# Kernel optimization log

Measured on AMD Instinct MI355X. Metric: run time of the kernel, lower is better.

Reference implementation:

```python
import jax, jax.numpy as jnp
import numpy as np
import math

D = 64          # emb_size
R = 32          # num relations
MAX_LEN = 5000  # position table size
E = 30000       # num edges / relation instances
EPSILON = 0.01
THETA = 0.01


def _build_Q():
    # sinusoidal axes [MAX_LEN, D]
    position = jnp.arange(MAX_LEN, dtype=jnp.float32)[:, None]
    div_term = jnp.exp(jnp.arange(0, D, 2, dtype=jnp.float32) * (-math.log(10000.0) / D))
    axes = jnp.zeros((MAX_LEN, D), dtype=jnp.float32)
    axes = axes.at[:, 0::2].set(jnp.sin(position * div_term))
    axes = axes.at[:, 1::2].set(jnp.cos(position * div_term))
    # skew-symmetric generator S_ij = theta * (a_i - a_j); Q = expm(S)  [MAX_LEN, D, D]
    S = THETA * (axes[..., None] - axes[:, None, :])
    Q = jax.scipy.linalg.expm(S)
    return Q


def setup_inputs() -> dict:
    key = jax.random.key(0)
    k1, k2, k3, k4, k5 = jax.random.split(key, 5)
    std = 1.0 / jnp.sqrt(jnp.float32(D))
    relation_embs = jax.random.normal(k1, (R, D, D), dtype=jnp.float32) * std
    Q = _build_Q()
    relation_mapping = jax.random.randint(k2, (E, 2), 0, 2 * R, dtype=jnp.int64 if jax.config.jax_enable_x64 else jnp.int32)
    node_mapping = jax.random.randint(k3, (MAX_LEN,), 0, MAX_LEN)
    edge_index = jax.random.randint(k4, (2, E), 0, MAX_LEN)
    node_embs = jax.random.normal(k5, (MAX_LEN, D), dtype=jnp.float32)
    return {
        "relation_mapping": relation_mapping,
        "node_mapping": node_mapping,
        "edge_index": edge_index,
        "node_embs": node_embs,
        "relation_embs": relation_embs,
        "Q": Q,
    }


def reference(relation_mapping, node_mapping, edge_index, node_embs, relation_embs, Q):
    # node_mapping, edge_index, node_embs are unused by the original forward
    I = jnp.eye(D, dtype=relation_embs.dtype)
    W_even = I + EPSILON * relation_embs   # [R, D, D]
    W_odd = I - EPSILON * relation_embs    # [R, D, D]
    # interleave -> W[2r] = W_even[r], W[2r+1] = W_odd[r]   [2R, D, D]
    W = jnp.stack([W_even, W_odd], axis=1).reshape(-1, D, D)
    Qg = Q[relation_mapping[:, 0]]         # [E, D, D] gather
    rel = W[relation_mapping[:, 1]]        # [E, D, D] gather
    # Q^T @ rel @ Q per edge
    out = jnp.einsum('eji,ejk,ekl->eil', Qg, rel, Qg)
    return out  # dropout p=0.0 is identity
```

## Files before the change

kernel.cpp:

```cpp
#include <hip/hip_runtime.h>

#define TRE_EPS    0.01f
#define TRE_CAP    256
#define TRE_NB     2048
#define TRE_T      8
#define TRE_NCHUNK 4

typedef float tre_f4 __attribute__((ext_vector_type(4)));
typedef short tre_bf8 __attribute__((ext_vector_type(8)));

__device__ __forceinline__ unsigned short tre_f2bf(float f) {
    unsigned int u = __float_as_uint(f);
    u += 0x7fffu + ((u >> 16) & 1u);
    return (unsigned short)(u >> 16);
}
__device__ __forceinline__ unsigned long long tre_pack4(float a, float b,
                                                        float c, float d) {
    return (unsigned long long)tre_f2bf(a)
         | ((unsigned long long)tre_f2bf(b) << 16)
         | ((unsigned long long)tre_f2bf(c) << 32)
         | ((unsigned long long)tre_f2bf(d) << 48);
}

__global__ __launch_bounds__(256) void tre_bin(
    const int* __restrict__ rm, int E,
    int* __restrict__ counts, int* __restrict__ list)
{
    int e = blockIdx.x * 256 + threadIdx.x;
    if (e >= E) return;
    int g  = rm[2 * e + 0];
    int r2 = rm[2 * e + 1];
    int b  = (g << 5) | (r2 >> 1);
    int idx = atomicAdd(&counts[b], 1);
    if (idx < TRE_CAP)
        list[b * TRE_CAP + idx] = (e << 1) | (r2 & 1);
}

__global__ __launch_bounds__(256) void tre_pair(
    const float* __restrict__ Q, const float* __restrict__ RE,
    const int* __restrict__ counts, const int* __restrict__ list,
    float* __restrict__ out)
{
    const int bb = blockIdx.x;
    const int b  = bb >> 2;
    const int c  = bb & 3;
    const int lo = c * TRE_T;

    const int cnt_raw = counts[b];
    const int cnt = cnt_raw > TRE_CAP ? TRE_CAP : cnt_raw;
    if (lo >= cnt) return;
    const int hi = (c < TRE_NCHUNK - 1) ? min(cnt, lo + TRE_T) : cnt;
    const int span = hi - lo;

    __shared__ __align__(16) unsigned char sB[16384];
    __shared__ int sList[TRE_CAP];

    const int g = b >> 5;
    const int r = b & 31;
    const int t = threadIdx.x;
    const int lane = t & 63;
    const int wv = t >> 6;
    const int fr = lane & 15;
    const int fq = lane >> 4;
    const int i0 = wv << 4;

    if (t < span) sList[t] = list[b * TRE_CAP + lo + t];

    const float* Qg  = Q  + ((size_t)g << 12);
    const float* REr = RE + ((size_t)r << 12);

    unsigned char* REb = sB;
    unsigned char* Qtb = sB + 8192;

    for (int i = t; i < 1024; i += 256) {
        float4 w = ((const float4*)REr)[i];
        int R = i >> 4, c0 = (i & 15) << 2;
        int o = c0 * 2;
        *(unsigned long long*)(REb + R * 128 + (o ^ ((R & 7) << 4))) =
            tre_pack4(w.x, w.y, w.z, w.w);
    }
    for (int it = 0; it < 4; ++it) {
        int k0 = (wv << 2) + (it << 4);
        float q0 = Qg[(k0 + 0) * 64 + lane];
        float q1 = Qg[(k0 + 1) * 64 + lane];
        float q2 = Qg[(k0 + 2) * 64 + lane];
        float q3 = Qg[(k0 + 3) * 64 + lane];
        int R = lane, o = k0 * 2;
        *(unsigned long long*)(Qtb + R * 128 + (o ^ ((R & 7) << 4))) =
            tre_pack4(q0, q1, q2, q3);
    }
    __syncthreads();

    tre_f4 accA[4];
#pragma unroll
    for (int jf = 0; jf < 4; ++jf) accA[jf] = (tre_f4){0.f, 0.f, 0.f, 0.f};
#pragma unroll
    for (int ks = 0; ks < 2; ++ks) {
        int ko = ks * 64 + fq * 16;
        int Ra = i0 + fr;
        tre_bf8 afr = *(const tre_bf8*)(REb + Ra * 128 + (ko ^ ((Ra & 7) << 4)));
#pragma unroll
        for (int jf = 0; jf < 4; ++jf) {
            int Rb = (jf << 4) + fr;
            tre_bf8 bfr = *(const tre_bf8*)(Qtb + Rb * 128 + (ko ^ ((Rb & 7) << 4)));
            accA[jf] = __builtin_amdgcn_mfma_f32_16x16x32_bf16(afr, bfr, accA[jf], 0, 0, 0);
        }
    }
    __syncthreads();

#pragma unroll
    for (int jf = 0; jf < 4; ++jf) {
        int C  = (jf << 4) + fr;
        int r0 = i0 + (fq << 2);
        int o  = r0 * 2;
        *(unsigned long long*)(sB + C * 128 + (o ^ ((C & 7) << 4))) =
            tre_pack4(accA[jf][0], accA[jf][1], accA[jf][2], accA[jf][3]);
    }
    __syncthreads();

    tre_f4 accM[4];
#pragma unroll
    for (int jf = 0; jf < 4; ++jf) accM[jf] = (tre_f4){0.f, 0.f, 0.f, 0.f};
#pragma unroll
    for (int ks = 0; ks < 2; ++ks) {
        int ko = ks * 64 + fq * 16;
        int Ra = i0 + fr;
        tre_bf8 afr = *(const tre_bf8*)(Qtb + Ra * 128 + (ko ^ ((Ra & 7) << 4)));
#pragma unroll
        for (int jf = 0; jf < 4; ++jf) {
            int Rb = (jf << 4) + fr;
            tre_bf8 bfr = *(const tre_bf8*)(sB + Rb * 128 + (ko ^ ((Rb & 7) << 4)));
            accM[jf] = __builtin_amdgcn_mfma_f32_16x16x32_bf16(afr, bfr, accM[jf], 0, 0, 0);
        }
    }
    __syncthreads();

    float* sM = (float*)sB;
#pragma unroll
    for (int jf = 0; jf < 4; ++jf) {
        int cc = (jf << 4) + fr;
        int r0 = i0 + (fq << 2);
        sM[(r0 + 0) * 64 + cc] = accM[jf][0];
        sM[(r0 + 1) * 64 + cc] = accM[jf][1];
        sM[(r0 + 2) * 64 + cc] = accM[jf][2];
        sM[(r0 + 3) * 64 + cc] = accM[jf][3];
    }
    __syncthreads();

    tre_f4 mreg[4], diag[4];
#pragma unroll
    for (int j = 0; j < 4; ++j) {
        mreg[j] = *(const tre_f4*)&sM[(t + 256 * j) << 2];
        int f = (t + 256 * j) << 2;
#pragma unroll
        for (int cc = 0; cc < 4; ++cc) {
            int fc = f + cc;
            diag[j][cc] = ((fc >> 6) == (fc & 63)) ? 1.0f : 0.0f;
        }
    }

    int pk = sList[0];
    for (int i = 0; i < span; ++i) {
        int nxt = (i + 1 < span) ? sList[i + 1] : 0;
        int e = pk >> 1;
        float s = (pk & 1) ? -TRE_EPS : TRE_EPS;
        tre_f4* dst = (tre_f4*)(out + ((size_t)e << 12));
#pragma unroll
        for (int j = 0; j < 4; ++j) {
            tre_f4 v = s * mreg[j] + diag[j];
            __builtin_nontemporal_store(v, &dst[t + 256 * j]);
        }
        pk = nxt;
    }
}

__global__ __launch_bounds__(256) void tre_direct(
    const int* __restrict__ rm, const float* __restrict__ Q,
    const float* __restrict__ RE, float* __restrict__ out)
{
    __shared__ float sQ[64 * 64];
    __shared__ float sW[64 * 65];

    const int e = blockIdx.x;
    const int g  = rm[2 * e + 0];
    const int r2 = rm[2 * e + 1];
    const int r  = r2 >> 1;
    const float s = (r2 & 1) ? -TRE_EPS : TRE_EPS;
    const int t = threadIdx.x;
    const int i0 = (t >> 4) << 2;
    const int l0 = (t & 15) << 2;

    const float* Qg  = Q  + ((size_t)g << 12);
    const float* REr = RE + ((size_t)r << 12);
    for (int i = t; i < 1024; i += 256) {
        ((float4*)sQ)[i] = ((const float4*)Qg)[i];
        float4 w = ((const float4*)REr)[i];
        int row = i >> 4, col = (i & 15) << 2;
        float* dst = &sW[row * 65 + col];
        dst[0] = w.x; dst[1] = w.y; dst[2] = w.z; dst[3] = w.w;
    }
    __syncthreads();

    float a[4][4] = {{0,0,0,0},{0,0,0,0},{0,0,0,0},{0,0,0,0}};
#pragma unroll 8
    for (int k = 0; k < 64; ++k) {
        float4 qv = *(const float4*)&sQ[(k << 6) + l0];
#pragma unroll
        for (int d = 0; d < 4; ++d) {
            float w = sW[(i0 + d) * 65 + k];
            a[d][0] = fmaf(w, qv.x, a[d][0]);
            a[d][1] = fmaf(w, qv.y, a[d][1]);
            a[d][2] = fmaf(w, qv.z, a[d][2]);
            a[d][3] = fmaf(w, qv.w, a[d][3]);
        }
    }
    __syncthreads();
    float* sA = sW;
#pragma unroll
    for (int d = 0; d < 4; ++d)
        *(float4*)&sA[(i0 + d) * 64 + l0] =
            make_float4(a[d][0], a[d][1], a[d][2], a[d][3]);
    __syncthreads();

    float qtq[4][4] = {{0,0,0,0},{0,0,0,0},{0,0,0,0},{0,0,0,0}};
    float qta[4][4] = {{0,0,0,0},{0,0,0,0},{0,0,0,0},{0,0,0,0}};
#pragma unroll 4
    for (int j = 0; j < 64; ++j) {
        float4 qi = *(const float4*)&sQ[(j << 6) + i0];
        float4 ql = *(const float4*)&sQ[(j << 6) + l0];
        float4 av = *(const float4*)&sA[(j << 6) + l0];
        float qiv[4] = {qi.x, qi.y, qi.z, qi.w};
        float qlv[4] = {ql.x, ql.y, ql.z, ql.w};
        float avv[4] = {av.x, av.y, av.z, av.w};
#pragma unroll
        for (int d = 0; d < 4; ++d)
#pragma unroll
            for (int ee = 0; ee < 4; ++ee) {
                qtq[d][ee] = fmaf(qiv[d], qlv[ee], qtq[d][ee]);
                qta[d][ee] = fmaf(qiv[d], avv[ee], qta[d][ee]);
            }
    }
    float* dst = out + ((size_t)e << 12);
#pragma unroll
    for (int d = 0; d < 4; ++d) {
        float4 v;
        v.x = fmaf(s, qta[d][0], qtq[d][0]);
        v.y = fmaf(s, qta[d][1], qtq[d][1]);
        v.z = fmaf(s, qta[d][2], qtq[d][2]);
        v.w = fmaf(s, qta[d][3], qtq[d][3]);
        *(float4*)&dst[(i0 + d) * 64 + l0] = v;
    }
}

extern "C" void kernel_launch(void* const* d_in, const int* in_sizes, int n_in,
                              void* d_out, int out_size, void* d_ws, size_t ws_size,
                              hipStream_t stream) {
    const int*   rm = (const int*)d_in[0];
    const float* RE = (const float*)d_in[4];
    const float* Q  = (const float*)d_in[5];
    float* out = (float*)d_out;
    const int E = in_sizes[0] / 2;

    const size_t cnt_bytes  = (size_t)TRE_NB * sizeof(int);
    const size_t list_bytes = (size_t)TRE_NB * TRE_CAP * sizeof(int);
    const size_t need = cnt_bytes + list_bytes;

    if (ws_size >= need) {
        int* counts = (int*)d_ws;
        int* list   = (int*)((char*)d_ws + cnt_bytes);
        hipMemsetAsync(counts, 0, cnt_bytes, stream);
        hipLaunchKernelGGL(tre_bin, dim3((E + 255) / 256), dim3(256), 0, stream,
                           rm, E, counts, list);
        hipLaunchKernelGGL(tre_pair, dim3(TRE_NB * TRE_NCHUNK), dim3(256), 0, stream,
                           Q, RE, counts, list, out);
    } else {
        hipLaunchKernelGGL(tre_direct, dim3(E), dim3(256), 0, stream,
                           rm, Q, RE, out);
    }
}
```

Measured before the change: 138.4 us.

## Compute per-bin transform once, cache as bf16, and fuse binning into it

The Q^T·RE·Q product for each (Q index, relation) bin was previously recomputed by every one of the four chunk blocks that write that bin's edges. Now a single block per bin computes it and stores the result as a bf16 tile in workspace. The same kernel also does the edge binning, replacing the separate bin kernel. A new lightweight gather kernel reads the tile, applies ±eps and the identity, and streams the outputs. This removes the redundant MFMA work and one launch, at the cost of an extra workspace round-trip and an additional bf16 rounding of the intermediate matrix.

```diff
diff --git a/kernel.cpp b/kernel.cpp
--- a/kernel.cpp
+++ b/kernel.cpp
@@ -8,11 +8,15 @@
 
 typedef float tre_f4 __attribute__((ext_vector_type(4)));
 typedef short tre_bf8 __attribute__((ext_vector_type(8)));
+typedef unsigned short tre_us8 __attribute__((ext_vector_type(8)));
 
 __device__ __forceinline__ unsigned short tre_f2bf(float f) {
     unsigned int u = __float_as_uint(f);
     u += 0x7fffu + ((u >> 16) & 1u);
     return (unsigned short)(u >> 16);
+}
+__device__ __forceinline__ float tre_bf2f(unsigned short u) {
+    return __uint_as_float(((unsigned int)u) << 16);
 }
 __device__ __forceinline__ unsigned long long tre_pack4(float a, float b,
                                                         float c, float d) {
@@ -22,53 +26,39 @@
          | ((unsigned long long)tre_f2bf(d) << 48);
 }
 
-__global__ __launch_bounds__(256) void tre_bin(
+__global__ __launch_bounds__(256) void tre_buildbin(
+    const float* __restrict__ Q, const float* __restrict__ RE,
     const int* __restrict__ rm, int E,
-    int* __restrict__ counts, int* __restrict__ list)
+    int* __restrict__ counts, int* __restrict__ list,
+    unsigned short* __restrict__ Tm)
 {
-    int e = blockIdx.x * 256 + threadIdx.x;
-    if (e >= E) return;
-    int g  = rm[2 * e + 0];
-    int r2 = rm[2 * e + 1];
-    int b  = (g << 5) | (r2 >> 1);
-    int idx = atomicAdd(&counts[b], 1);
-    if (idx < TRE_CAP)
-        list[b * TRE_CAP + idx] = (e << 1) | (r2 & 1);
-}
-
-__global__ __launch_bounds__(256) void tre_pair(
-    const float* __restrict__ Q, const float* __restrict__ RE,
-    const int* __restrict__ counts, const int* __restrict__ list,
-    float* __restrict__ out)
-{
-    const int bb = blockIdx.x;
-    const int b  = bb >> 2;
-    const int c  = bb & 3;
-    const int lo = c * TRE_T;
-
-    const int cnt_raw = counts[b];
-    const int cnt = cnt_raw > TRE_CAP ? TRE_CAP : cnt_raw;
-    if (lo >= cnt) return;
-    const int hi = (c < TRE_NCHUNK - 1) ? min(cnt, lo + TRE_T) : cnt;
-    const int span = hi - lo;
-
     __shared__ __align__(16) unsigned char sB[16384];
-    __shared__ int sList[TRE_CAP];
+
+    const int b = blockIdx.x;
+    const int t = threadIdx.x;
+
+    {
+        int e = b * 256 + t;
+        if (e < E) {
+            int g  = rm[2 * e + 0];
+            int r2 = rm[2 * e + 1];
+            int bk = (g << 5) | (r2 >> 1);
+            int idx = atomicAdd(&counts[bk], 1);
+            if (idx < TRE_CAP)
+                list[bk * TRE_CAP + idx] = (e << 1) | (r2 & 1);
+        }
+    }
 
     const int g = b >> 5;
     const int r = b & 31;
-    const int t = threadIdx.x;
     const int lane = t & 63;
     const int wv = t >> 6;
     const int fr = lane & 15;
     const int fq = lane >> 4;
     const int i0 = wv << 4;
 
-    if (t < span) sList[t] = list[b * TRE_CAP + lo + t];
-
     const float* Qg  = Q  + ((size_t)g << 12);
     const float* REr = RE + ((size_t)r << 12);
-
     unsigned char* REb = sB;
     unsigned char* Qtb = sB + 8192;
 
@@ -147,10 +137,46 @@
     }
     __syncthreads();
 
+    unsigned short* dst = Tm + ((size_t)b << 12);
+#pragma unroll
+    for (int jj = 0; jj < 2; ++jj) {
+        int u = t + 256 * jj;
+        const float* src = &sM[u << 3];
+        tre_us8 p;
+#pragma unroll
+        for (int c = 0; c < 8; ++c) p[c] = tre_f2bf(src[c]);
+        *(tre_us8*)(dst + (u << 3)) = p;
+    }
+}
+
+__global__ __launch_bounds__(256) void tre_gather(
+    const int* __restrict__ counts, const int* __restrict__ list,
+    const unsigned short* __restrict__ Tm, float* __restrict__ out)
+{
+    const int bb = blockIdx.x;
+    const int b  = bb >> 2;
+    const int c  = bb & 3;
+    const int lo = c * TRE_T;
+
+    const int cnt_raw = counts[b];
+    const int cnt = cnt_raw > TRE_CAP ? TRE_CAP : cnt_raw;
+    if (lo >= cnt) return;
+    const int hi = (c < TRE_NCHUNK - 1) ? min(cnt, lo + TRE_T) : cnt;
+    const int span = hi - lo;
+
+    __shared__ int sList[TRE_CAP];
+    const int t = threadIdx.x;
+    if (t < span) sList[t] = list[b * TRE_CAP + lo + t];
+
+    const ushort4* tile = (const ushort4*)(Tm + ((size_t)b << 12));
     tre_f4 mreg[4], diag[4];
 #pragma unroll
     for (int j = 0; j < 4; ++j) {
-        mreg[j] = *(const tre_f4*)&sM[(t + 256 * j) << 2];
+        ushort4 m4 = tile[t + 256 * j];
+        mreg[j][0] = tre_bf2f(m4.x);
+        mreg[j][1] = tre_bf2f(m4.y);
+        mreg[j][2] = tre_bf2f(m4.z);
+        mreg[j][3] = tre_bf2f(m4.w);
         int f = (t + 256 * j) << 2;
 #pragma unroll
         for (int cc = 0; cc < 4; ++cc) {
@@ -158,6 +184,7 @@
             diag[j][cc] = ((fc >> 6) == (fc & 63)) ? 1.0f : 0.0f;
         }
     }
+    __syncthreads();
 
     int pk = sList[0];
     for (int i = 0; i < span; ++i) {
@@ -263,16 +290,18 @@
 
     const size_t cnt_bytes  = (size_t)TRE_NB * sizeof(int);
     const size_t list_bytes = (size_t)TRE_NB * TRE_CAP * sizeof(int);
-    const size_t need = cnt_bytes + list_bytes;
+    const size_t tm_bytes   = (size_t)TRE_NB * 4096 * sizeof(unsigned short);
+    const size_t need = cnt_bytes + list_bytes + tm_bytes;
 
     if (ws_size >= need) {
         int* counts = (int*)d_ws;
         int* list   = (int*)((char*)d_ws + cnt_bytes);
+        unsigned short* Tm = (unsigned short*)((char*)d_ws + cnt_bytes + list_bytes);
         hipMemsetAsync(counts, 0, cnt_bytes, stream);
-        hipLaunchKernelGGL(tre_bin, dim3((E + 255) / 256), dim3(256), 0, stream,
-                           rm, E, counts, list);
-        hipLaunchKernelGGL(tre_pair, dim3(TRE_NB * TRE_NCHUNK), dim3(256), 0, stream,
-                           Q, RE, counts, list, out);
+        hipLaunchKernelGGL(tre_buildbin, dim3(TRE_NB), dim3(256), 0, stream,
+                           Q, RE, rm, E, counts, list, Tm);
+        hipLaunchKernelGGL(tre_gather, dim3(TRE_NB * TRE_NCHUNK), dim3(256), 0, stream,
+                           counts, list, Tm, out);
     } else {
         hipLaunchKernelGGL(tre_direct, dim3(E), dim3(256), 0, stream,
                            rm, Q, RE, out);
```

Measured after the change: 152.0 us. 9.9% more time.
